# Performance work log

Hardware: AMD Instinct MI355X
Metric: run time of the kernel (lower is better)

The kernel has to match this reference:

```python
import jax, jax.numpy as jnp
import numpy as np

N = 100000
E = 2000000
F = 64          # in_features == out_features (required by attention * h_j)
BETA = 0.5
NEG_SLOPE = 0.01  # torch F.leaky_relu default


def setup_inputs() -> dict:
    key = jax.random.key(0)
    k1, k2, k3, k4, k5, k6 = jax.random.split(key, 6)
    h = jax.random.normal(k1, (N, F), dtype=jnp.float32)
    adj = jax.random.randint(k2, (2, E), 0, N, dtype=jnp.int64)
    amount = jax.random.uniform(k3, (E,), dtype=jnp.float32)
    count = jax.random.uniform(k4, (E,), dtype=jnp.float32)
    fc_w = jax.random.normal(k5, (F, 2 * F), dtype=jnp.float32) * (1.0 / np.sqrt(2 * F))
    fc_b = jax.random.normal(k6, (F,), dtype=jnp.float32) * 0.01
    return {"h": h, "adj": adj, "amount": amount, "count": count,
            "fc_w": fc_w, "fc_b": fc_b}


def _minmax_norm(x):
    lo, hi = x.min(), x.max()
    return (x - lo) / (hi - lo + 1e-8)


def reference(h, adj, amount, count, fc_w, fc_b):
    # per-edge weight from normalized amount/count
    edge_weight = BETA * _minmax_norm(amount) + (1.0 - BETA) * _minmax_norm(count)  # [E]

    src, dst = adj[0], adj[1]
    h_i = h[src]                     # [E, F]
    h_j = h[dst]                     # [E, F]
    h_cat = jnp.concatenate([h_i, h_j], axis=1)  # [E, 2F]

    score = jnp.einsum('ef,of->eo', h_cat, fc_w) + fc_b  # [E, F_out]
    score = jnp.where(score >= 0, score, NEG_SLOPE * score)  # leaky_relu
    score = score * edge_weight[:, None]

    # softmax over ALL edges (dim 0), per feature, as in the original
    attention = jax.nn.softmax(score, axis=0)  # [E, F]

    agg = jnp.zeros_like(h).at[src].add(attention * h_j)  # scatter-add -> [N, F]
    return agg
```

## Files before the change

### kernel.cpp

```cpp
#include <hip/hip_runtime.h>
#include <hip/hip_fp16.h>
#include <math.h>

#define FDIM   64
#define NB     64
#define BSHIFT 7
#define BMASK  127
#define CHUNKA 4096
#define CHUNKM 2048
#define CAP    3072
#define CAPB   3584

__global__ __launch_bounds__(256) void mp_k(const float* __restrict__ amount,
                                            const float* __restrict__ count,
                                            float4* __restrict__ partial,
                                            const float* __restrict__ h,
                                            const float* __restrict__ fc_w,
                                            const float* __restrict__ fc_b,
                                            float* __restrict__ G1,
                                            __half2* __restrict__ P,
                                            int E, int N, int nblkM) {
  __shared__ float hs[NB * FDIM];
  const int t = threadIdx.x;
  if (blockIdx.x < nblkM) {
    float amin = 3.4e38f, amax = -3.4e38f, cmin = 3.4e38f, cmax = -3.4e38f;
    int e0 = blockIdx.x * CHUNKM + t * 8;
    if (e0 + 8 <= E) {
      #pragma unroll
      for (int q = 0; q < 8; q += 4) {
        float4 a4 = *(const float4*)(amount + e0 + q);
        float4 c4 = *(const float4*)(count + e0 + q);
        amin = fminf(amin, fminf(fminf(a4.x, a4.y), fminf(a4.z, a4.w)));
        amax = fmaxf(amax, fmaxf(fmaxf(a4.x, a4.y), fmaxf(a4.z, a4.w)));
        cmin = fminf(cmin, fminf(fminf(c4.x, c4.y), fminf(c4.z, c4.w)));
        cmax = fmaxf(cmax, fmaxf(fmaxf(c4.x, c4.y), fmaxf(c4.z, c4.w)));
      }
    } else {
      for (int e = e0; e < E; e++) {
        float a = amount[e], c = count[e];
        amin = fminf(amin, a); amax = fmaxf(amax, a);
        cmin = fminf(cmin, c); cmax = fmaxf(cmax, c);
      }
    }
    #pragma unroll
    for (int off = 32; off; off >>= 1) {
      amin = fminf(amin, __shfl_down(amin, off));
      amax = fmaxf(amax, __shfl_down(amax, off));
      cmin = fminf(cmin, __shfl_down(cmin, off));
      cmax = fmaxf(cmax, __shfl_down(cmax, off));
    }
    float4* lred = (float4*)hs;
    if ((t & 63) == 0) lred[t >> 6] = make_float4(amin, amax, cmin, cmax);
    __syncthreads();
    if (t == 0) {
      float4 r = lred[0];
      #pragma unroll
      for (int w = 1; w < 4; w++) {
        r.x = fminf(r.x, lred[w].x); r.y = fmaxf(r.y, lred[w].y);
        r.z = fminf(r.z, lred[w].z); r.w = fmaxf(r.w, lred[w].w);
      }
      partial[blockIdx.x] = r;
    }
  } else {
    const int pgb = blockIdx.x - nblkM;
    const int o = t & 63;
    const int grp = t >> 6;
    const int half = grp & 1;
    const int rh = grp >> 1;
    float w[FDIM];
    const float* wrow = fc_w + o * 128 + half * 64;
    #pragma unroll
    for (int f = 0; f < FDIM; f += 4) {
      float4 v = *(const float4*)(wrow + f);
      w[f] = v.x; w[f + 1] = v.y; w[f + 2] = v.z; w[f + 3] = v.w;
    }
    const float bias = (half == 0) ? fc_b[o] : 0.0f;
    const int n0 = pgb * NB;
    const int nrows = min(NB, N - n0);
    for (int i = t; i < nrows * FDIM; i += 256) hs[i] = h[(size_t)n0 * FDIM + i];
    __syncthreads();
    const int r0 = rh * (NB / 2);
    const int r1 = min(r0 + NB / 2, nrows);
    for (int n = r0; n < r1; n++) {
      float4 a4 = make_float4(0.f, 0.f, 0.f, 0.f);
      #pragma unroll
      for (int f = 0; f < FDIM; f += 4) {
        float4 hv = *(const float4*)(&hs[n * FDIM + f]);
        a4.x += hv.x * w[f];
        a4.y += hv.y * w[f + 1];
        a4.z += hv.z * w[f + 2];
        a4.w += hv.w * w[f + 3];
      }
      float acc = (a4.x + a4.y) + (a4.z + a4.w) + bias;
      if (half == 0) {
        G1[(size_t)(n0 + n) * FDIM + o] = acc;
      } else {
        P[(size_t)(n0 + n) * FDIM + o] =
            __halves2half2(__float2half(acc), __float2half(hs[n * FDIM + o]));
      }
    }
  }
}

__global__ __launch_bounds__(256) void init_k(const float4* __restrict__ partial,
                                              int nb, float* __restrict__ mmf,
                                              int* __restrict__ cursor, int nbkt,
                                              double* __restrict__ colsum) {
  int t = threadIdx.x;
  for (int k = t; k < nbkt; k += 256) cursor[k] = k * CAPB;
  for (int i = t; i < 1024; i += 256) colsum[i] = 0.0;
  float amin = 3.4e38f, amax = -3.4e38f, cmin = 3.4e38f, cmax = -3.4e38f;
  for (int i = t; i < nb; i += 256) {
    float4 p = partial[i];
    amin = fminf(amin, p.x); amax = fmaxf(amax, p.y);
    cmin = fminf(cmin, p.z); cmax = fmaxf(cmax, p.w);
  }
  #pragma unroll
  for (int off = 32; off; off >>= 1) {
    amin = fminf(amin, __shfl_down(amin, off));
    amax = fmaxf(amax, __shfl_down(amax, off));
    cmin = fminf(cmin, __shfl_down(cmin, off));
    cmax = fmaxf(cmax, __shfl_down(cmax, off));
  }
  __shared__ float4 lred[4];
  if ((t & 63) == 0) lred[t >> 6] = make_float4(amin, amax, cmin, cmax);
  __syncthreads();
  if (t == 0) {
    float4 r = lred[0];
    #pragma unroll
    for (int w = 1; w < 4; w++) {
      r.x = fminf(r.x, lred[w].x); r.y = fmaxf(r.y, lred[w].y);
      r.z = fminf(r.z, lred[w].z); r.w = fmaxf(r.w, lred[w].w);
    }
    mmf[0] = r.x; mmf[1] = r.y; mmf[2] = r.z; mmf[3] = r.w;
  }
}

__global__ __launch_bounds__(256) void scatter_k(const int* __restrict__ src,
                                                 const int* __restrict__ dst,
                                                 const float* __restrict__ amount,
                                                 const float* __restrict__ count,
                                                 const float* __restrict__ mmf,
                                                 int* __restrict__ cursor,
                                                 int2* __restrict__ payload,
                                                 int E, int nbkt) {
  __shared__ int cntb[1024];
  __shared__ int baseb[1024];
  __shared__ int sbase[1024];
  __shared__ int wsum[4];
  __shared__ int2 lpay[CHUNKA];
  __shared__ unsigned short lbkt[CHUNKA];
  const int t = threadIdx.x, blk = blockIdx.x;
  for (int k = t; k < nbkt; k += 256) cntb[k] = 0;
  __syncthreads();
  const float amin = mmf[0], amax = mmf[1], cmin = mmf[2], cmax = mmf[3];
  const float L2E = 1.4426950408889634f;
  const float ascale = 0.5f * L2E / (amax - amin + 1e-8f);
  const float cscale = 0.5f * L2E / (cmax - cmin + 1e-8f);
  int e0 = blk * CHUNKA + t * 16;
  const bool full = (e0 + 16 <= E);
  int4 S[4]; int4 D[4]; float4 A[4]; float4 C[4];
  if (full) {
    #pragma unroll
    for (int q = 0; q < 4; q++) {
      S[q] = *(const int4*)(src + e0 + 4 * q);
      D[q] = *(const int4*)(dst + e0 + 4 * q);
      A[q] = *(const float4*)(amount + e0 + 4 * q);
      C[q] = *(const float4*)(count + e0 + 4 * q);
      atomicAdd(&cntb[S[q].x >> BSHIFT], 1);
      atomicAdd(&cntb[S[q].y >> BSHIFT], 1);
      atomicAdd(&cntb[S[q].z >> BSHIFT], 1);
      atomicAdd(&cntb[S[q].w >> BSHIFT], 1);
    }
  } else {
    for (int e = e0; e < E; e++) atomicAdd(&cntb[src[e] >> BSHIFT], 1);
  }
  __syncthreads();
  {
    const int wv = t >> 6, ln = t & 63;
    int carry = 0;
    #pragma unroll
    for (int c = 0; c < 4; c++) {
      int idx = (wv << 8) + (c << 6) + ln;
      int x = (idx < nbkt) ? cntb[idx] : 0;
      int v = x;
      #pragma unroll
      for (int off = 1; off < 64; off <<= 1) {
        int u = __shfl_up(v, off);
        if (ln >= off) v += u;
      }
      if (idx < nbkt) baseb[idx] = carry + v - x;
      carry += __shfl(v, 63);
    }
    if (ln == 0) wsum[wv] = carry;
  }
  __syncthreads();
  {
    const int wv = t >> 6, ln = t & 63;
    int wpre = 0;
    #pragma unroll
    for (int i = 0; i < 4; i++) wpre += (i < wv) ? wsum[i] : 0;
    if (wpre) {
      #pragma unroll
      for (int c = 0; c < 4; c++) {
        int idx = (wv << 8) + (c << 6) + ln;
        if (idx < nbkt) baseb[idx] += wpre;
      }
    }
  }
  __syncthreads();
  for (int k = t; k < nbkt; k += 256) {
    int cnt = cntb[k];
    if (cnt) sbase[k] = atomicAdd(&cursor[k], cnt);
    cntb[k] = baseb[k];
  }
  __syncthreads();
  auto ins = [&](int s, int d, float a, float c) {
    int b = s >> BSHIFT;
    float ew = (a - amin) * ascale + (c - cmin) * cscale;
    int pos = atomicAdd(&cntb[b], 1);
    lpay[pos] = make_int2((d << 8) | (s & BMASK), __float_as_int(ew));
    lbkt[pos] = (unsigned short)b;
  };
  if (full) {
    #pragma unroll
    for (int q = 0; q < 4; q++) {
      ins(S[q].x, D[q].x, A[q].x, C[q].x);
      ins(S[q].y, D[q].y, A[q].y, C[q].y);
      ins(S[q].z, D[q].z, A[q].z, C[q].z);
      ins(S[q].w, D[q].w, A[q].w, C[q].w);
    }
  } else {
    for (int e = e0; e < E; e++) ins(src[e], dst[e], amount[e], count[e]);
  }
  __syncthreads();
  const int ned = min(CHUNKA, E - blk * CHUNKA);
  for (int i = t; i < ned; i += 256) {
    int bk = lbkt[i];
    int gpos = sbase[bk] + (i - baseb[bk]);
    if (gpos < (bk + 1) * CAPB)
      payload[gpos] = lpay[i];
  }
}

__device__ __forceinline__ float2 unpack_h2(unsigned u) {
  __half2 v = *(__half2*)&u;
  return make_float2(__low2float(v), __high2float(v));
}

__global__ __launch_bounds__(512) void fusedB_k(const int2* __restrict__ payload,
                                                const int* __restrict__ cursor,
                                                const float* __restrict__ G1,
                                                const unsigned* __restrict__ P,
                                                double* __restrict__ colsum,
                                                float* __restrict__ out,
                                                int E, int nbkt) {
  __shared__ int2 lpay[CAP];
  __shared__ int fcnt[128];
  __shared__ int fcur[128];
  __shared__ float part[512];
  const int b = blockIdx.x;
  const int t = threadIdx.x;
  const int lane = t & 63;
  const int wv = __builtin_amdgcn_readfirstlane(t >> 6);
  const int node0 = b << BSHIFT;
  const int base = b * CAPB;
  int end = cursor[b];
  if (end > base + CAPB) end = base + CAPB;
  const int nchunks = (end - base + CAP - 1) / CAP;
  const bool multi = (nchunks > 1);
  float csum = 0.0f;
  for (int c = 0; c < nchunks; c++) {
    const int cs = base + c * CAP;
    const int m = min(CAP, end - cs);
    if (t < 128) fcnt[t] = 0;
    __syncthreads();
    int2 myp0, myp1, myp2, myp3, myp4, myp5;
    {
      int i;
      i = t;        if (i < m) { myp0 = payload[cs + i]; atomicAdd(&fcnt[myp0.x & 127], 1); }
      i = t + 512;  if (i < m) { myp1 = payload[cs + i]; atomicAdd(&fcnt[myp1.x & 127], 1); }
      i = t + 1024; if (i < m) { myp2 = payload[cs + i]; atomicAdd(&fcnt[myp2.x & 127], 1); }
      i = t + 1536; if (i < m) { myp3 = payload[cs + i]; atomicAdd(&fcnt[myp3.x & 127], 1); }
      i = t + 2048; if (i < m) { myp4 = payload[cs + i]; atomicAdd(&fcnt[myp4.x & 127], 1); }
      i = t + 2560; if (i < m) { myp5 = payload[cs + i]; atomicAdd(&fcnt[myp5.x & 127], 1); }
    }
    __syncthreads();
    if (wv == 0) {
      int carry = 0;
      #pragma unroll
      for (int cc = 0; cc < 2; cc++) {
        int idx = (cc << 6) + lane;
        int x = fcnt[idx];
        int v = x;
        #pragma unroll
        for (int off = 1; off < 64; off <<= 1) {
          int u = __shfl_up(v, off);
          if (lane >= off) v += u;
        }
        fcur[idx] = carry + v - x;
        carry += __shfl(v, 63);
      }
    }
    __syncthreads();
    {
      int i;
      i = t;        if (i < m) lpay[atomicAdd(&fcur[myp0.x & 127], 1)] = myp0;
      i = t + 512;  if (i < m) lpay[atomicAdd(&fcur[myp1.x & 127], 1)] = myp1;
      i = t + 1024; if (i < m) lpay[atomicAdd(&fcur[myp2.x & 127], 1)] = myp2;
      i = t + 1536; if (i < m) lpay[atomicAdd(&fcur[myp3.x & 127], 1)] = myp3;
      i = t + 2048; if (i < m) lpay[atomicAdd(&fcur[myp4.x & 127], 1)] = myp4;
      i = t + 2560; if (i < m) lpay[atomicAdd(&fcur[myp5.x & 127], 1)] = myp5;
    }
    __syncthreads();
    const int per = (((m + 7) >> 3) + 63) & ~63;
    const int ws = wv * per;
    const int we = min(ws + per, m);
    int curnode = -1;
    bool firstf = true;
    float acc = 0.0f, g1 = 0.0f;
    auto flush_to = [&](int node) {
      if (curnode >= 0) {
        float* dp = out + (size_t)curnode * FDIM + lane;
        if (multi || firstf) { atomicAdd(dp, acc); firstf = false; }
        else *dp = acc;
      }
      curnode = node; acc = 0.0f;
      g1 = G1[(size_t)node * FDIM + lane];
    };
    for (int c0 = ws; c0 < we; c0 += 64) {
      const int mm = min(64, we - c0);
      int2 p = make_int2(0, 0);
      if (lane < mm) p = lpay[c0 + lane];
      if (mm == 64) {
        #pragma unroll 1
        for (int j = 0; j < 64; j += 16) {
          int xs[16]; float ee[16]; unsigned uu[16];
          #pragma unroll
          for (int k = 0; k < 16; k++) {
            xs[k] = __builtin_amdgcn_readlane(p.x, j + k);
            ee[k] = __int_as_float(__builtin_amdgcn_readlane(p.y, j + k));
          }
          #pragma unroll
          for (int k = 0; k < 16; k++) {
            unsigned off = (((unsigned)xs[k]) & 0xFFFFFF00u) | ((unsigned)lane << 2);
            uu[k] = *(const unsigned*)((const char*)P + off);
          }
          #pragma unroll
          for (int k = 0; k < 16; k++) {
            int node = node0 + (xs[k] & 127);
            if (node != curnode) flush_to(node);
            float2 v = unpack_h2(uu[k]);
            float sc = g1 + v.x;
            sc = fmaxf(sc, 0.01f * sc);
            float x = exp2f(sc * ee[k]);
            csum += x;
            acc += x * v.y;
          }
        }
      } else {
        for (int j = 0; j < mm; j += 16) {
          const int rem = mm - j;
          int xs[16]; float ee[16]; unsigned uu[16];
          #pragma unroll
          for (int k = 0; k < 16; k++) {
            xs[k] = __builtin_amdgcn_readlane(p.x, j + k);
            ee[k] = __int_as_float(__builtin_amdgcn_readlane(p.y, j + k));
          }
          #pragma unroll
          for (int k = 0; k < 16; k++) {
            unsigned off = (((unsigned)xs[k]) & 0xFFFFFF00u) | ((unsigned)lane << 2);
            uu[k] = *(const unsigned*)((const char*)P + off);
          }
          #pragma unroll
          for (int k = 0; k < 16; k++) {
            if (k < rem) {
              int node = node0 + (xs[k] & 127);
              if (node != curnode) flush_to(node);
              float2 v = unpack_h2(uu[k]);
              float sc = g1 + v.x;
              sc = fmaxf(sc, 0.01f * sc);
              float x = exp2f(sc * ee[k]);
              csum += x;
              acc += x * v.y;
            }
          }
        }
      }
    }
    if (curnode >= 0) atomicAdd(out + (size_t)curnode * FDIM + lane, acc);
    __syncthreads();
  }
  part[t] = csum;
  __syncthreads();
  if (t < 64) {
    float tot = 0.0f;
    #pragma unroll
    for (int w = 0; w < 8; w++) tot += part[t + (w << 6)];
    atomicAdd(&colsum[t * 16], (double)tot);
  }
}

__global__ __launch_bounds__(256) void scale_k(float4* __restrict__ out4,
                                               const double* __restrict__ colsum,
                                               int total4) {
  __shared__ float rinv_s[64];
  if (threadIdx.x < 64) rinv_s[threadIdx.x] = (float)(1.0 / colsum[threadIdx.x * 16]);
  __syncthreads();
  const float4* r4 = (const float4*)rinv_s;
  int idx = blockIdx.x * blockDim.x + threadIdx.x;
  int stride = gridDim.x * blockDim.x;
  for (int i = idx; i < total4; i += stride) {
    float4 v = out4[i];
    float4 r = r4[i & 15];
    v.x *= r.x; v.y *= r.y; v.z *= r.z; v.w *= r.w;
    out4[i] = v;
  }
}

extern "C" void kernel_launch(void* const* d_in, const int* in_sizes, int n_in,
                              void* d_out, int out_size, void* d_ws, size_t ws_size,
                              hipStream_t stream) {
  const float* h      = (const float*)d_in[0];
  const int*   adj    = (const int*)d_in[1];
  const float* amount = (const float*)d_in[2];
  const float* count  = (const float*)d_in[3];
  const float* fc_w   = (const float*)d_in[4];
  const float* fc_b   = (const float*)d_in[5];
  float* out = (float*)d_out;

  const int E = in_sizes[2];
  const int N = in_sizes[0] / FDIM;
  const int* src = adj;
  const int* dst = adj + E;
  const int nbkt  = (N + BMASK) >> BSHIFT;
  const int nblkA = (E + CHUNKA - 1) / CHUNKA;
  const int nblkM = (E + CHUNKM - 1) / CHUNKM;
  const int npg   = (N + NB - 1) / NB;

  char* ws = (char*)d_ws;
  size_t off = 0;
  auto alloc = [&](size_t bytes) { void* p = ws + off; off += (bytes + 255) & ~(size_t)255; return p; };
  float*    G1      = (float*)alloc((size_t)N * FDIM * sizeof(float));
  __half2*  P       = (__half2*)alloc((size_t)N * FDIM * sizeof(__half2));
  int2*     payload = (int2*)alloc((size_t)nbkt * CAPB * sizeof(int2));
  int*      cursor  = (int*)alloc(1024 * sizeof(int));
  float4*   mmpart  = (float4*)alloc((size_t)nblkM * sizeof(float4));
  double*   colsum  = (double*)alloc(1024 * sizeof(double));
  float*    mmf     = (float*)alloc(4 * sizeof(float));

  mp_k<<<nblkM + npg, 256, 0, stream>>>(amount, count, mmpart, h, fc_w, fc_b,
                                        G1, P, E, N, nblkM);
  init_k<<<1, 256, 0, stream>>>(mmpart, nblkM, mmf, cursor, nbkt, colsum);
  scatter_k<<<nblkA, 256, 0, stream>>>(src, dst, amount, count, mmf, cursor, payload, E, nbkt);
  fusedB_k<<<nbkt, 512, 0, stream>>>(payload, cursor, G1, (const unsigned*)P, colsum, out, E, nbkt);
  scale_k<<<1024, 256, 0, stream>>>((float4*)out, colsum, N * FDIM / 4);
}
```

Baseline: 279.8 us.

## Halve source-node bucket width to double fusedB blocks and shrink scatter chunk

Buckets now cover 64 source nodes instead of 128, so there are about 1563 buckets and fusedB launches twice as many smaller blocks with smaller shared staging buffers. The scatter kernel processes 3072 edges per block, extends its bucket prefix scan to 1792 entries, and folds the global cursor base into baseb to drop the sbase array. The aim is better occupancy and load balance in the aggregation kernel. In exchange, scatter_k does more global cursor atomics and a longer scan per block, and there are more partial-output atomics at bucket boundaries. init_k still appears to reset cursor for nbkt entries, which now exceeds the 1024 used before, so correctness depends on that hidden code handling the larger count.

```diff
diff --git a/kernel.cpp b/kernel.cpp
--- a/kernel.cpp
+++ b/kernel.cpp
@@ -4,12 +4,13 @@
 
 #define FDIM   64
 #define NB     64
-#define BSHIFT 7
-#define BMASK  127
-#define CHUNKA 4096
+#define BSHIFT 6
+#define BMASK  63
+#define NBKT_AL 1792
+#define CHUNKA 3072
 #define CHUNKM 2048
-#define CAP    3072
-#define CAPB   3584
+#define CAP    1792
+#define CAPB   2048
 
 __global__ __launch_bounds__(256) void mp_k(const float* __restrict__ amount,
                                             const float* __restrict__ count,
@@ -144,9 +145,8 @@
                                                  int* __restrict__ cursor,
                                                  int2* __restrict__ payload,
                                                  int E, int nbkt) {
-  __shared__ int cntb[1024];
-  __shared__ int baseb[1024];
-  __shared__ int sbase[1024];
+  __shared__ int cntb[NBKT_AL];
+  __shared__ int baseb[NBKT_AL];
   __shared__ int wsum[4];
   __shared__ int2 lpay[CHUNKA];
   __shared__ unsigned short lbkt[CHUNKA];
@@ -157,12 +157,12 @@
   const float L2E = 1.4426950408889634f;
   const float ascale = 0.5f * L2E / (amax - amin + 1e-8f);
   const float cscale = 0.5f * L2E / (cmax - cmin + 1e-8f);
-  int e0 = blk * CHUNKA + t * 16;
-  const bool full = (e0 + 16 <= E);
-  int4 S[4]; int4 D[4]; float4 A[4]; float4 C[4];
+  int e0 = blk * CHUNKA + t * 12;
+  const bool full = (e0 + 12 <= E);
+  int4 S[3]; int4 D[3]; float4 A[3]; float4 C[3];
   if (full) {
     #pragma unroll
-    for (int q = 0; q < 4; q++) {
+    for (int q = 0; q < 3; q++) {
       S[q] = *(const int4*)(src + e0 + 4 * q);
       D[q] = *(const int4*)(dst + e0 + 4 * q);
       A[q] = *(const float4*)(amount + e0 + 4 * q);
@@ -180,8 +180,8 @@
     const int wv = t >> 6, ln = t & 63;
     int carry = 0;
     #pragma unroll
-    for (int c = 0; c < 4; c++) {
-      int idx = (wv << 8) + (c << 6) + ln;
+    for (int c = 0; c < 7; c++) {
+      int idx = wv * 448 + (c << 6) + ln;
       int x = (idx < nbkt) ? cntb[idx] : 0;
       int v = x;
       #pragma unroll
@@ -202,8 +202,8 @@
     for (int i = 0; i < 4; i++) wpre += (i < wv) ? wsum[i] : 0;
     if (wpre) {
       #pragma unroll
-      for (int c = 0; c < 4; c++) {
-        int idx = (wv << 8) + (c << 6) + ln;
+      for (int c = 0; c < 7; c++) {
+        int idx = wv * 448 + (c << 6) + ln;
         if (idx < nbkt) baseb[idx] += wpre;
       }
     }
@@ -211,8 +211,12 @@
   __syncthreads();
   for (int k = t; k < nbkt; k += 256) {
     int cnt = cntb[k];
-    if (cnt) sbase[k] = atomicAdd(&cursor[k], cnt);
-    cntb[k] = baseb[k];
+    int bb = baseb[k];
+    cntb[k] = bb;
+    if (cnt) {
+      int sb = atomicAdd(&cursor[k], cnt);
+      baseb[k] = sb - bb;
+    }
   }
   __syncthreads();
   auto ins = [&](int s, int d, float a, float c) {
@@ -224,7 +228,7 @@
   };
   if (full) {
     #pragma unroll
-    for (int q = 0; q < 4; q++) {
+    for (int q = 0; q < 3; q++) {
       ins(S[q].x, D[q].x, A[q].x, C[q].x);
       ins(S[q].y, D[q].y, A[q].y, C[q].y);
       ins(S[q].z, D[q].z, A[q].z, C[q].z);
@@ -237,7 +241,7 @@
   const int ned = min(CHUNKA, E - blk * CHUNKA);
   for (int i = t; i < ned; i += 256) {
     int bk = lbkt[i];
-    int gpos = sbase[bk] + (i - baseb[bk]);
+    int gpos = baseb[bk] + i;
     if (gpos < (bk + 1) * CAPB)
       payload[gpos] = lpay[i];
   }
@@ -256,8 +260,8 @@
                                                 float* __restrict__ out,
                                                 int E, int nbkt) {
   __shared__ int2 lpay[CAP];
-  __shared__ int fcnt[128];
-  __shared__ int fcur[128];
+  __shared__ int fcnt[64];
+  __shared__ int fcur[64];
   __shared__ float part[512];
   const int b = blockIdx.x;
   const int t = threadIdx.x;
@@ -273,44 +277,34 @@
   for (int c = 0; c < nchunks; c++) {
     const int cs = base + c * CAP;
     const int m = min(CAP, end - cs);
-    if (t < 128) fcnt[t] = 0;
-    __syncthreads();
-    int2 myp0, myp1, myp2, myp3, myp4, myp5;
+    if (t < 64) fcnt[t] = 0;
+    __syncthreads();
+    int2 myp0, myp1, myp2, myp3;
     {
       int i;
-      i = t;        if (i < m) { myp0 = payload[cs + i]; atomicAdd(&fcnt[myp0.x & 127], 1); }
-      i = t + 512;  if (i < m) { myp1 = payload[cs + i]; atomicAdd(&fcnt[myp1.x & 127], 1); }
-      i = t + 1024; if (i < m) { myp2 = payload[cs + i]; atomicAdd(&fcnt[myp2.x & 127], 1); }
-      i = t + 1536; if (i < m) { myp3 = payload[cs + i]; atomicAdd(&fcnt[myp3.x & 127], 1); }
-      i = t + 2048; if (i < m) { myp4 = payload[cs + i]; atomicAdd(&fcnt[myp4.x & 127], 1); }
-      i = t + 2560; if (i < m) { myp5 = payload[cs + i]; atomicAdd(&fcnt[myp5.x & 127], 1); }
+      i = t;        if (i < m) { myp0 = payload[cs + i]; atomicAdd(&fcnt[myp0.x & 63], 1); }
+      i = t + 512;  if (i < m) { myp1 = payload[cs + i]; atomicAdd(&fcnt[myp1.x & 63], 1); }
+      i = t + 1024; if (i < m) { myp2 = payload[cs + i]; atomicAdd(&fcnt[myp2.x & 63], 1); }
+      i = t + 1536; if (i < m) { myp3 = payload[cs + i]; atomicAdd(&fcnt[myp3.x & 63], 1); }
     }
     __syncthreads();
     if (wv == 0) {
-      int carry = 0;
-      #pragma unroll
-      for (int cc = 0; cc < 2; cc++) {
-        int idx = (cc << 6) + lane;
-        int x = fcnt[idx];
-        int v = x;
-        #pragma unroll
-        for (int off = 1; off < 64; off <<= 1) {
-          int u = __shfl_up(v, off);
-          if (lane >= off) v += u;
-        }
-        fcur[idx] = carry + v - x;
-        carry += __shfl(v, 63);
-      }
+      int x = fcnt[lane];
+      int v = x;
+      #pragma unroll
+      for (int off = 1; off < 64; off <<= 1) {
+        int u = __shfl_up(v, off);
+        if (lane >= off) v += u;
+      }
+      fcur[lane] = v - x;
     }
     __syncthreads();
     {
       int i;
-      i = t;        if (i < m) lpay[atomicAdd(&fcur[myp0.x & 127], 1)] = myp0;
-      i = t + 512;  if (i < m) lpay[atomicAdd(&fcur[myp1.x & 127], 1)] = myp1;
-      i = t + 1024; if (i < m) lpay[atomicAdd(&fcur[myp2.x & 127], 1)] = myp2;
-      i = t + 1536; if (i < m) lpay[atomicAdd(&fcur[myp3.x & 127], 1)] = myp3;
-      i = t + 2048; if (i < m) lpay[atomicAdd(&fcur[myp4.x & 127], 1)] = myp4;
-      i = t + 2560; if (i < m) lpay[atomicAdd(&fcur[myp5.x & 127], 1)] = myp5;
+      i = t;        if (i < m) lpay[atomicAdd(&fcur[myp0.x & 63], 1)] = myp0;
+      i = t + 512;  if (i < m) lpay[atomicAdd(&fcur[myp1.x & 63], 1)] = myp1;
+      i = t + 1024; if (i < m) lpay[atomicAdd(&fcur[myp2.x & 63], 1)] = myp2;
+      i = t + 1536; if (i < m) lpay[atomicAdd(&fcur[myp3.x & 63], 1)] = myp3;
     }
     __syncthreads();
     const int per = (((m + 7) >> 3) + 63) & ~63;
@@ -348,7 +342,7 @@
           }
           #pragma unroll
           for (int k = 0; k < 16; k++) {
-            int node = node0 + (xs[k] & 127);
+            int node = node0 + (xs[k] & 63);
             if (node != curnode) flush_to(node);
             float2 v = unpack_h2(uu[k]);
             float sc = g1 + v.x;
@@ -375,7 +369,7 @@
           #pragma unroll
           for (int k = 0; k < 16; k++) {
             if (k < rem) {
-              int node = node0 + (xs[k] & 127);
+              int node = node0 + (xs[k] & 63);
               if (node != curnode) flush_to(node);
               float2 v = unpack_h2(uu[k]);
               float sc = g1 + v.x;
@@ -444,7 +438,7 @@
   float*    G1      = (float*)alloc((size_t)N * FDIM * sizeof(float));
   __half2*  P       = (__half2*)alloc((size_t)N * FDIM * sizeof(__half2));
   int2*     payload = (int2*)alloc((size_t)nbkt * CAPB * sizeof(int2));
-  int*      cursor  = (int*)alloc(1024 * sizeof(int));
+  int*      cursor  = (int*)alloc((size_t)NBKT_AL * sizeof(int));
   float4*   mmpart  = (float4*)alloc((size_t)nblkM * sizeof(float4));
   double*   colsum  = (double*)alloc(1024 * sizeof(double));
   float*    mmf     = (float*)alloc(4 * sizeof(float));
```

Result: no change. 276.2 us (-1.3%).
